# Kernel optimization log

Hardware: AMD Instinct MI355X
Metric: run time of the kernel (lower is better)

The kernel has to match this reference:

```python
import jax, jax.numpy as jnp
import numpy as np

N_NODES = 50000
N_EDGES = 800000
IN_FEATS = 256
HIDDEN = 256
NUM_CLASSES = 64


def setup_inputs() -> dict:
    key = jax.random.key(0)
    k1, k2, k3, k4 = jax.random.split(key, 4)
    features = jax.random.normal(k1, (N_NODES, IN_FEATS), dtype=jnp.float32)
    edge_index = jax.random.randint(k2, (2, N_EDGES), 0, N_NODES, dtype=jnp.int32)
    W1 = jax.random.normal(k3, (IN_FEATS, HIDDEN), dtype=jnp.float32) * (1.0 / np.sqrt(IN_FEATS))
    b1 = jnp.zeros((HIDDEN,), dtype=jnp.float32)
    W2 = jax.random.normal(k4, (HIDDEN, NUM_CLASSES), dtype=jnp.float32) * (1.0 / np.sqrt(HIDDEN))
    b2 = jnp.zeros((NUM_CLASSES,), dtype=jnp.float32)
    return {"features": features, "edge_index": edge_index, "W1": W1, "b1": b1, "W2": W2, "b2": b2}


def reference(features, edge_index, W1, b1, W2, b2):
    # Two-layer GCN: h = A_hat @ relu(A_hat @ X W1 + b1) W2 + b2
    # A_hat uses symmetric degree normalization 1/sqrt(d_src * d_dst)
    N = features.shape[0]
    src, dst = edge_index[0], edge_index[1]
    ones = jnp.ones((src.shape[0],), dtype=features.dtype)
    deg_out = jax.ops.segment_sum(ones, src, num_segments=N)  # out-degree per node
    deg_in = jax.ops.segment_sum(ones, dst, num_segments=N)   # in-degree per node
    inv_sqrt_out = jax.lax.rsqrt(jnp.maximum(deg_out, 1.0))
    inv_sqrt_in = jax.lax.rsqrt(jnp.maximum(deg_in, 1.0))
    edge_norm = (inv_sqrt_out[src] * inv_sqrt_in[dst])[:, None]  # [E,1]

    def gcn_layer(x, W, b):
        h = x @ W                      # transform first (reduces message width)
        msg = h[src] * edge_norm       # [E, out]
        agg = jax.ops.segment_sum(msg, dst, num_segments=N)
        return agg + b

    h = jax.nn.relu(gcn_layer(features, W1, b1))
    return gcn_layer(h, W2, b2)
```

## Files before the change

### kernel.cpp

```cpp
#include <hip/hip_runtime.h>

#define NN 50000
#define MPAD 50048
#define NE 800000
#define SCAN_BLOCKS 49

typedef short short8 __attribute__((ext_vector_type(8)));
typedef float f32x4 __attribute__((ext_vector_type(4)));

__device__ __forceinline__ unsigned short f2bf(float x) {
    unsigned u = __builtin_bit_cast(unsigned, x);
    u += 0x7FFFu + ((u >> 16) & 1u);
    return (unsigned short)(u >> 16);
}
__device__ __forceinline__ float bf2f(unsigned short h) {
    unsigned u = ((unsigned)h) << 16;
    return __builtin_bit_cast(float, u);
}
__device__ __forceinline__ void gld16(const void* g, void* l) {
    __builtin_amdgcn_global_load_lds(
        (const __attribute__((address_space(1))) unsigned int*)g,
        (__attribute__((address_space(3))) unsigned int*)l, 16, 0, 0);
}
__device__ __forceinline__ void nt_store8(void* p, ushort4 v) {
    __builtin_nontemporal_store(__builtin_bit_cast(unsigned long long, v),
                                (unsigned long long*)p);
}


__global__ __launch_bounds__(256) void count_kernel(const int* __restrict__ src,
    const int* __restrict__ dst, int* __restrict__ cnt_out, int* __restrict__ cnt_in, int E)
{
    int e = blockIdx.x * 256 + threadIdx.x;
    if (e < E) {
        atomicAdd(&cnt_out[src[e]], 1);
        atomicAdd(&cnt_in[dst[e]], 1);
    }
}

__global__ __launch_bounds__(256) void scanA_kernel(const int* __restrict__ cnt,
    int* __restrict__ bsum)
{
    __shared__ int sm[256];
    int b = blockIdx.x, tid = threadIdx.x;
    int base = b * 1024 + tid * 4;
    int s = 0;
    #pragma unroll
    for (int i = 0; i < 4; ++i) {
        int idx = base + i;
        if (idx < NN) s += cnt[idx];
    }
    sm[tid] = s;
    __syncthreads();
    for (int off = 128; off > 0; off >>= 1) {
        if (tid < off) sm[tid] += sm[tid + off];
        __syncthreads();
    }
    if (tid == 0) bsum[b] = sm[0];
}

__global__ __launch_bounds__(64) void scanB_kernel(const int* __restrict__ bsum,
    int* __restrict__ bexcl)
{
    int tid = threadIdx.x;
    int orig = (tid < SCAN_BLOCKS) ? bsum[tid] : 0;
    int v = orig;
    #pragma unroll
    for (int off = 1; off < 64; off <<= 1) {
        int u = __shfl_up(v, off, 64);
        if (tid >= off) v += u;
    }
    if (tid < SCAN_BLOCKS) bexcl[tid] = v - orig;
}

__global__ __launch_bounds__(256) void scanC_kernel(const int* __restrict__ cnt,
    const int* __restrict__ cnt_out, const int* __restrict__ bexcl,
    int* __restrict__ rs, float* __restrict__ inv_out, float* __restrict__ inv_in)
{
    __shared__ int wsum[4];
    int b = blockIdx.x, tid = threadIdx.x;
    int lane = tid & 63, wv = tid >> 6;
    int base = b * 1024 + tid * 4;
    int v[4]; int s = 0;
    #pragma unroll
    for (int i = 0; i < 4; ++i) {
        int idx = base + i;
        v[i] = (idx < NN) ? cnt[idx] : 0;
        s += v[i];
    }
    int inc = s;
    #pragma unroll
    for (int off = 1; off < 64; off <<= 1) {
        int u = __shfl_up(inc, off, 64);
        if (lane >= off) inc += u;
    }
    if (lane == 63) wsum[wv] = inc;
    __syncthreads();
    int wo = 0;
    for (int i = 0; i < wv; ++i) wo += wsum[i];
    int run = wo + (inc - s) + bexcl[b];
    #pragma unroll
    for (int i = 0; i < 4; ++i) {
        int idx = base + i;
        if (idx < NN) {
            rs[idx] = run; run += v[i];
            inv_in[idx]  = rsqrtf(fmaxf((float)v[i], 1.0f));
            inv_out[idx] = rsqrtf(fmaxf((float)cnt_out[idx], 1.0f));
        }
    }
}

__global__ __launch_bounds__(256) void fill_kernel(const int* __restrict__ src,
    const int* __restrict__ dst, int* __restrict__ rs, int* __restrict__ csr_src, int E)
{
    int e = blockIdx.x * 256 + threadIdx.x;
    if (e < E) {
        int slot = atomicAdd(&rs[dst[e]], 1);
        csr_src[slot] = src[e];
    }
}

__global__ __launch_bounds__(256) void splitX_kernel(const float* __restrict__ X,
    unsigned short* __restrict__ Xh, unsigned short* __restrict__ Xl)
{
    int i = blockIdx.x * 256 + threadIdx.x;
    if (i >= NN * 32) return;
    int r = i >> 5, c = i & 31;
    const float* src = X + (size_t)r * 256 + c * 8;
    float4 a0 = *(const float4*)src;
    float4 a1 = *(const float4*)(src + 4);
    float xs[8] = {a0.x, a0.y, a0.z, a0.w, a1.x, a1.y, a1.z, a1.w};
    short8 hv, lv;
    #pragma unroll
    for (int t = 0; t < 8; ++t) {
        unsigned short h = f2bf(xs[t]);
        hv[t] = (short)h;
        lv[t] = (short)f2bf(xs[t] - bf2f(h));
    }
    size_t off = (size_t)r * 256 + (c >> 3) * 64 + (((c & 7) ^ (r & 7)) * 8);
    *(short8*)&Xh[off] = hv;
    *(short8*)&Xl[off] = lv;
}

__global__ __launch_bounds__(256) void splitW_kernel(const float* __restrict__ W1,
    const float* __restrict__ W2, unsigned short* __restrict__ W1T,
    unsigned short* __restrict__ W2T)
{
    int i = blockIdx.x * 256 + threadIdx.x;
    const float* W; unsigned short* BT; int N; int ii;
    if (i < 256 * 32) { W = W1; BT = W1T; N = 256; ii = i; }
    else if (i < 256 * 32 + 64 * 32) { W = W2; BT = W2T; N = 64; ii = i - 256 * 32; }
    else return;
    int col = ii >> 5, kc = ii & 31;
    #pragma unroll
    for (int j = 0; j < 8; ++j) {
        float x = W[(size_t)(kc * 8 + j) * N + col];
        unsigned short h = f2bf(x);
        BT[(size_t)col * 512 + kc * 8 + j] = h;
        BT[(size_t)col * 512 + 256 + kc * 8 + j] = f2bf(x - bf2f(h));
    }
}

template<int BN>
__global__ __launch_bounds__(256) void gemm_sp_kernel(
    const unsigned short* __restrict__ Ah, const unsigned short* __restrict__ Al,
    const unsigned short* __restrict__ BT, const float* __restrict__ inv_out,
    unsigned short* __restrict__ C, int M, int Ntot)
{
    constexpr int WN = BN / 2;
    constexpr int NF = WN / 16;
    __shared__ unsigned short Ash[128 * 64];
    __shared__ unsigned short Asl[128 * 64];
    const int tid = threadIdx.x;
    const int w = tid >> 6, lane = tid & 63;
    const int wm = w >> 1, wn = w & 1;
    const int r = lane & 15, kg = lane >> 4;
    const int rowbase = blockIdx.x * 128;
    const int colbase = blockIdx.y * BN;

    f32x4 acc[4][NF] = {};

    for (int kb = 0; kb < 4; ++kb) {
        #pragma unroll
        for (int i = 0; i < 4; ++i) {
            int ct = (w * 4 + i) * 64 + lane;
            int row = ct >> 3, c = ct & 7;
            size_t goff = (size_t)(rowbase + row) * 256 + kb * 64 + c * 8;
            gld16(Ah + goff, (unsigned short*)Ash + (size_t)ct * 8);
            gld16(Al + goff, (unsigned short*)Asl + (size_t)ct * 8);
        }
        __syncthreads();
        #pragma unroll
        for (int ks = 0; ks < 2; ++ks) {
            short8 ahf[4], alf[4];
            #pragma unroll
            for (int mf = 0; mf < 4; ++mf) {
                int row = wm * 64 + mf * 16 + r;
                int lo = row * 64 + (((ks * 4 + kg) ^ (row & 7)) * 8);
                ahf[mf] = *(const short8*)&Ash[lo];
                alf[mf] = *(const short8*)&Asl[lo];
            }
            #pragma unroll
            for (int nf = 0; nf < NF; ++nf) {
                const unsigned short* bp = BT
                    + (size_t)(colbase + wn * WN + nf * 16 + r) * 512
                    + kb * 64 + ks * 32 + kg * 8;
                short8 bh = *(const short8*)bp;
                short8 bl = *(const short8*)(bp + 256);
                #pragma unroll
                for (int mf = 0; mf < 4; ++mf) {
                    acc[mf][nf] = __builtin_amdgcn_mfma_f32_16x16x32_bf16(ahf[mf], bh, acc[mf][nf], 0, 0, 0);
                    acc[mf][nf] = __builtin_amdgcn_mfma_f32_16x16x32_bf16(alf[mf], bh, acc[mf][nf], 0, 0, 0);
                    acc[mf][nf] = __builtin_amdgcn_mfma_f32_16x16x32_bf16(ahf[mf], bl, acc[mf][nf], 0, 0, 0);
                }
            }
        }
        __syncthreads();
    }

    #pragma unroll
    for (int mf = 0; mf < 4; ++mf) {
        #pragma unroll
        for (int reg = 0; reg < 4; ++reg) {
            int orow = rowbase + wm * 64 + mf * 16 + kg * 4 + reg;
            if (orow >= M) continue;
            float sc = inv_out[orow];
            #pragma unroll
            for (int nf = 0; nf < NF; ++nf) {
                int ocol = colbase + wn * WN + nf * 16 + r;
                C[(size_t)orow * Ntot + ocol] = f2bf(acc[mf][nf][reg] * sc);
            }
        }
    }
}

__global__ __launch_bounds__(256) void gather256_kernel(const unsigned short* __restrict__ t1,
    const int* __restrict__ csr_src, const int* __restrict__ rs,
    const float* __restrict__ inv_in, const float* __restrict__ b1,
    unsigned short* __restrict__ Ah2, unsigned short* __restrict__ Al2)
{
    int n = (int)((blockIdx.x * 256 + threadIdx.x) >> 6);
    int lane = threadIdx.x & 63;
    if (n >= NN) return;
    int begin = (n == 0) ? 0 : rs[n - 1];
    int end = rs[n];
    float a0 = 0.f, a1 = 0.f, a2 = 0.f, a3 = 0.f;
    int j = begin;
    for (; j + 8 <= end; j += 8) {
        int s0 = csr_src[j],     s1 = csr_src[j + 1], s2 = csr_src[j + 2], s3 = csr_src[j + 3];
        int s4 = csr_src[j + 4], s5 = csr_src[j + 5], s6 = csr_src[j + 6], s7 = csr_src[j + 7];
        ushort4 v0 = *(const ushort4*)&t1[(size_t)s0 * 256 + lane * 4];
        ushort4 v1 = *(const ushort4*)&t1[(size_t)s1 * 256 + lane * 4];
        ushort4 v2 = *(const ushort4*)&t1[(size_t)s2 * 256 + lane * 4];
        ushort4 v3 = *(const ushort4*)&t1[(size_t)s3 * 256 + lane * 4];
        ushort4 v4 = *(const ushort4*)&t1[(size_t)s4 * 256 + lane * 4];
        ushort4 v5 = *(const ushort4*)&t1[(size_t)s5 * 256 + lane * 4];
        ushort4 v6 = *(const ushort4*)&t1[(size_t)s6 * 256 + lane * 4];
        ushort4 v7 = *(const ushort4*)&t1[(size_t)s7 * 256 + lane * 4];
        a0 += bf2f(v0.x); a1 += bf2f(v0.y); a2 += bf2f(v0.z); a3 += bf2f(v0.w);
        a0 += bf2f(v1.x); a1 += bf2f(v1.y); a2 += bf2f(v1.z); a3 += bf2f(v1.w);
        a0 += bf2f(v2.x); a1 += bf2f(v2.y); a2 += bf2f(v2.z); a3 += bf2f(v2.w);
        a0 += bf2f(v3.x); a1 += bf2f(v3.y); a2 += bf2f(v3.z); a3 += bf2f(v3.w);
        a0 += bf2f(v4.x); a1 += bf2f(v4.y); a2 += bf2f(v4.z); a3 += bf2f(v4.w);
        a0 += bf2f(v5.x); a1 += bf2f(v5.y); a2 += bf2f(v5.z); a3 += bf2f(v5.w);
        a0 += bf2f(v6.x); a1 += bf2f(v6.y); a2 += bf2f(v6.z); a3 += bf2f(v6.w);
        a0 += bf2f(v7.x); a1 += bf2f(v7.y); a2 += bf2f(v7.z); a3 += bf2f(v7.w);
    }
    for (; j < end; ++j) {
        int s = csr_src[j];
        ushort4 v = *(const ushort4*)&t1[(size_t)s * 256 + lane * 4];
        a0 += bf2f(v.x); a1 += bf2f(v.y); a2 += bf2f(v.z); a3 += bf2f(v.w);
    }
    float win = inv_in[n];
    int f0 = lane * 4;
    float4 bb = *(const float4*)&b1[f0];
    float x0 = fmaxf(fmaf(a0, win, bb.x), 0.f);
    float x1 = fmaxf(fmaf(a1, win, bb.y), 0.f);
    float x2 = fmaxf(fmaf(a2, win, bb.z), 0.f);
    float x3 = fmaxf(fmaf(a3, win, bb.w), 0.f);
    unsigned short h0 = f2bf(x0), h1 = f2bf(x1), h2 = f2bf(x2), h3 = f2bf(x3);
    ushort4 hv = {h0, h1, h2, h3};
    ushort4 lv = {f2bf(x0 - bf2f(h0)), f2bf(x1 - bf2f(h1)),
                  f2bf(x2 - bf2f(h2)), f2bf(x3 - bf2f(h3))};
    int kb = f0 >> 6, c = (f0 >> 3) & 7, e = f0 & 7;
    size_t off = (size_t)n * 256 + kb * 64 + ((c ^ (n & 7)) * 8) + e;
    nt_store8(&Ah2[off], hv);
    nt_store8(&Al2[off], lv);
}

__global__ __launch_bounds__(256) void gather64_kernel(const unsigned short* __restrict__ t2,
    const int* __restrict__ csr_src, const int* __restrict__ rs,
    const float* __restrict__ inv_in, const float* __restrict__ b2,
    float* __restrict__ out)
{
    int n = (int)((blockIdx.x * 256 + threadIdx.x) >> 6);
    int lane = threadIdx.x & 63;
    if (n >= NN) return;
    int begin = (n == 0) ? 0 : rs[n - 1];
    int end = rs[n];
    float acc = 0.f;
    int j = begin;
    for (; j + 8 <= end; j += 8) {
        int s0 = csr_src[j],     s1 = csr_src[j + 1], s2 = csr_src[j + 2], s3 = csr_src[j + 3];
        int s4 = csr_src[j + 4], s5 = csr_src[j + 5], s6 = csr_src[j + 6], s7 = csr_src[j + 7];
        float v0 = bf2f(t2[(size_t)s0 * 64 + lane]);
        float v1 = bf2f(t2[(size_t)s1 * 64 + lane]);
        float v2 = bf2f(t2[(size_t)s2 * 64 + lane]);
        float v3 = bf2f(t2[(size_t)s3 * 64 + lane]);
        float v4 = bf2f(t2[(size_t)s4 * 64 + lane]);
        float v5 = bf2f(t2[(size_t)s5 * 64 + lane]);
        float v6 = bf2f(t2[(size_t)s6 * 64 + lane]);
        float v7 = bf2f(t2[(size_t)s7 * 64 + lane]);
        acc += v0; acc += v1; acc += v2; acc += v3;
        acc += v4; acc += v5; acc += v6; acc += v7;
    }
    for (; j < end; ++j) {
        int s = csr_src[j];
        acc += bf2f(t2[(size_t)s * 64 + lane]);
    }
    float o = fmaf(acc, inv_in[n], b2[lane]);
    __builtin_nontemporal_store(o, &out[(size_t)n * 64 + lane]);
}

extern "C" void kernel_launch(void* const* d_in, const int* in_sizes, int n_in,
                              void* d_out, int out_size, void* d_ws, size_t ws_size,
                              hipStream_t stream)
{
    const float* features = (const float*)d_in[0];
    const int*   edge_index = (const int*)d_in[1];
    const float* W1 = (const float*)d_in[2];
    const float* b1 = (const float*)d_in[3];
    const float* W2 = (const float*)d_in[4];
    const float* b2 = (const float*)d_in[5];
    float* out = (float*)d_out;
    const int* src = edge_index;
    const int* dst = edge_index + NE;

    char* p = (char*)d_ws;
    int* cnt_out = (int*)p;            p += (size_t)NN * 4;
    int* cnt_in  = (int*)p;            p += (size_t)NN * 4;
    float* inv_out = (float*)p;        p += (size_t)NN * 4;
    float* inv_in  = (float*)p;        p += (size_t)NN * 4;
    int* rs      = (int*)p;            p += (size_t)NN * 4;
    int* csr_src = (int*)p;            p += (size_t)NE * 4;
    int* bsum    = (int*)p;            p += 64 * 4;
    int* bexcl   = (int*)p;            p += 64 * 4;
    unsigned short* W1T = (unsigned short*)p;  p += (size_t)256 * 512 * 2;
    unsigned short* W2T = (unsigned short*)p;  p += (size_t)64 * 512 * 2;
    unsigned short* Xh  = (unsigned short*)p;  p += (size_t)MPAD * 256 * 2;
    unsigned short* Xl  = (unsigned short*)p;  p += (size_t)MPAD * 256 * 2;
    unsigned short* t1  = (unsigned short*)p;  p += (size_t)NN * 256 * 2;
    unsigned short* Ah2 = (unsigned short*)p;  p += (size_t)MPAD * 256 * 2;
    unsigned short* Al2 = (unsigned short*)p;  p += (size_t)MPAD * 256 * 2;
    unsigned short* t2  = (unsigned short*)p;  p += (size_t)NN * 64 * 2;

    hipMemsetAsync(cnt_out, 0, 2 * (size_t)NN * sizeof(int), stream);

    count_kernel<<<(NE + 255) / 256, 256, 0, stream>>>(src, dst, cnt_out, cnt_in, NE);
    scanA_kernel<<<SCAN_BLOCKS, 256, 0, stream>>>(cnt_in, bsum);
    scanB_kernel<<<1, 64, 0, stream>>>(bsum, bexcl);
    scanC_kernel<<<SCAN_BLOCKS, 256, 0, stream>>>(cnt_in, cnt_out, bexcl, rs, inv_out, inv_in);
    fill_kernel<<<(NE + 255) / 256, 256, 0, stream>>>(src, dst, rs, csr_src, NE);

    splitX_kernel<<<(NN * 32 + 255) / 256, 256, 0, stream>>>(features, Xh, Xl);
    splitW_kernel<<<(320 * 32 + 255) / 256, 256, 0, stream>>>(W1, W2, W1T, W2T);

    gemm_sp_kernel<128><<<dim3(MPAD / 128, 2), 256, 0, stream>>>(
        Xh, Xl, W1T, inv_out, t1, NN, 256);

    gather256_kernel<<<(NN * 64 + 255) / 256, 256, 0, stream>>>(
        t1, csr_src, rs, inv_in, b1, Ah2, Al2);

    gemm_sp_kernel<64><<<dim3(MPAD / 128, 1), 256, 0, stream>>>(
        Ah2, Al2, W2T, inv_out, t2, NN, 64);

    gather64_kernel<<<(NN * 64 + 255) / 256, 256, 0, stream>>>(
        t2, csr_src, rs, inv_in, b2, out);
}
```

Before: 340.6 us.

## Fuse fp32-to-bf16 split of X into first GEMM and stage B in LDS

The separate splitX pass, which wrote hi/lo bf16 copies of the features to global memory, is removed. The first GEMM now loads fp32 rows directly, splits them into hi/lo in registers and writes them swizzled into LDS. Both GEMMs also stage the swizzled transposed weight tiles in LDS instead of reading B fragments straight from global memory each k-step. This cuts a full write and re-read of a large intermediate buffer plus one launch, at the cost of more LDS per block and synchronous register-path loads for A in GEMM1.

New measurement: 300.6 us. -11.7%, faster.

```diff
diff --git a/kernel.cpp b/kernel.cpp
--- a/kernel.cpp
+++ b/kernel.cpp
@@ -120,28 +120,6 @@
     }
 }
 
-__global__ __launch_bounds__(256) void splitX_kernel(const float* __restrict__ X,
-    unsigned short* __restrict__ Xh, unsigned short* __restrict__ Xl)
-{
-    int i = blockIdx.x * 256 + threadIdx.x;
-    if (i >= NN * 32) return;
-    int r = i >> 5, c = i & 31;
-    const float* src = X + (size_t)r * 256 + c * 8;
-    float4 a0 = *(const float4*)src;
-    float4 a1 = *(const float4*)(src + 4);
-    float xs[8] = {a0.x, a0.y, a0.z, a0.w, a1.x, a1.y, a1.z, a1.w};
-    short8 hv, lv;
-    #pragma unroll
-    for (int t = 0; t < 8; ++t) {
-        unsigned short h = f2bf(xs[t]);
-        hv[t] = (short)h;
-        lv[t] = (short)f2bf(xs[t] - bf2f(h));
-    }
-    size_t off = (size_t)r * 256 + (c >> 3) * 64 + (((c & 7) ^ (r & 7)) * 8);
-    *(short8*)&Xh[off] = hv;
-    *(short8*)&Xl[off] = lv;
-}
-
 __global__ __launch_bounds__(256) void splitW_kernel(const float* __restrict__ W1,
     const float* __restrict__ W2, unsigned short* __restrict__ W1T,
     unsigned short* __restrict__ W2T)
@@ -152,25 +130,29 @@
     else if (i < 256 * 32 + 64 * 32) { W = W2; BT = W2T; N = 64; ii = i - 256 * 32; }
     else return;
     int col = ii >> 5, kc = ii & 31;
+    short8 hv, lv;
     #pragma unroll
     for (int j = 0; j < 8; ++j) {
         float x = W[(size_t)(kc * 8 + j) * N + col];
         unsigned short h = f2bf(x);
-        BT[(size_t)col * 512 + kc * 8 + j] = h;
-        BT[(size_t)col * 512 + 256 + kc * 8 + j] = f2bf(x - bf2f(h));
-    }
-}
-
-template<int BN>
-__global__ __launch_bounds__(256) void gemm_sp_kernel(
-    const unsigned short* __restrict__ Ah, const unsigned short* __restrict__ Al,
+        hv[j] = (short)h;
+        lv[j] = (short)f2bf(x - bf2f(h));
+    }
+    size_t base = (size_t)col * 512;
+    size_t o = (kc >> 3) * 64 + (((kc & 7) ^ (col & 7)) * 8);
+    *(short8*)&BT[base + o] = hv;
+    *(short8*)&BT[base + 256 + o] = lv;
+}
+
+__global__ __launch_bounds__(256) void gemm1_fuse_kernel(const float* __restrict__ X,
     const unsigned short* __restrict__ BT, const float* __restrict__ inv_out,
-    unsigned short* __restrict__ C, int M, int Ntot)
-{
-    constexpr int WN = BN / 2;
-    constexpr int NF = WN / 16;
+    unsigned short* __restrict__ C, int M)
+{
+    constexpr int BN = 128, WN = 64, NF = 4;
     __shared__ unsigned short Ash[128 * 64];
     __shared__ unsigned short Asl[128 * 64];
+    __shared__ unsigned short Bsh[BN * 64];
+    __shared__ unsigned short Bsl[BN * 64];
     const int tid = threadIdx.x;
     const int w = tid >> 6, lane = tid & 63;
     const int wm = w >> 1, wn = w & 1;
@@ -185,9 +167,29 @@
         for (int i = 0; i < 4; ++i) {
             int ct = (w * 4 + i) * 64 + lane;
             int row = ct >> 3, c = ct & 7;
-            size_t goff = (size_t)(rowbase + row) * 256 + kb * 64 + c * 8;
-            gld16(Ah + goff, (unsigned short*)Ash + (size_t)ct * 8);
-            gld16(Al + goff, (unsigned short*)Asl + (size_t)ct * 8);
+            int grow = rowbase + row; if (grow >= NN) grow = NN - 1;
+            const float* sp = X + (size_t)grow * 256 + kb * 64 + c * 8;
+            float4 x0 = *(const float4*)sp;
+            float4 x1 = *(const float4*)(sp + 4);
+            float xs[8] = {x0.x, x0.y, x0.z, x0.w, x1.x, x1.y, x1.z, x1.w};
+            short8 hv, lv;
+            #pragma unroll
+            for (int t = 0; t < 8; ++t) {
+                unsigned short h = f2bf(xs[t]);
+                hv[t] = (short)h;
+                lv[t] = (short)f2bf(xs[t] - bf2f(h));
+            }
+            int dsto = row * 64 + ((c ^ (row & 7)) * 8);
+            *(short8*)&Ash[dsto] = hv;
+            *(short8*)&Asl[dsto] = lv;
+        }
+        #pragma unroll
+        for (int i = 0; i < 4; ++i) {
+            int ct = (w * 4 + i) * 64 + lane;
+            int col = ct >> 3, c = ct & 7;
+            size_t goff = (size_t)(colbase + col) * 512 + kb * 64 + c * 8;
+            gld16(BT + goff, (unsigned short*)Bsh + (size_t)ct * 8);
+            gld16(BT + goff + 256, (unsigned short*)Bsl + (size_t)ct * 8);
         }
         __syncthreads();
         #pragma unroll
@@ -202,11 +204,10 @@
             }
             #pragma unroll
             for (int nf = 0; nf < NF; ++nf) {
-                const unsigned short* bp = BT
-                    + (size_t)(colbase + wn * WN + nf * 16 + r) * 512
-                    + kb * 64 + ks * 32 + kg * 8;
-                short8 bh = *(const short8*)bp;
-                short8 bl = *(const short8*)(bp + 256);
+                int col = wn * WN + nf * 16 + r;
+                int lo = col * 64 + (((ks * 4 + kg) ^ (col & 7)) * 8);
+                short8 bh = *(const short8*)&Bsh[lo];
+                short8 bl = *(const short8*)&Bsl[lo];
                 #pragma unroll
                 for (int mf = 0; mf < 4; ++mf) {
                     acc[mf][nf] = __builtin_amdgcn_mfma_f32_16x16x32_bf16(ahf[mf], bh, acc[mf][nf], 0, 0, 0);
@@ -228,7 +229,86 @@
             #pragma unroll
             for (int nf = 0; nf < NF; ++nf) {
                 int ocol = colbase + wn * WN + nf * 16 + r;
-                C[(size_t)orow * Ntot + ocol] = f2bf(acc[mf][nf][reg] * sc);
+                C[(size_t)orow * 256 + ocol] = f2bf(acc[mf][nf][reg] * sc);
+            }
+        }
+    }
+}
+
+__global__ __launch_bounds__(256) void gemm2_kernel(
+    const unsigned short* __restrict__ Ah, const unsigned short* __restrict__ Al,
+    const unsigned short* __restrict__ BT, const float* __restrict__ inv_out,
+    unsigned short* __restrict__ C, int M)
+{
+    constexpr int BN = 64, WN = 32, NF = 2, BI = 2;
+    __shared__ unsigned short Ash[128 * 64];
+    __shared__ unsigned short Asl[128 * 64];
+    __shared__ unsigned short Bsh[BN * 64];
+    __shared__ unsigned short Bsl[BN * 64];
+    const int tid = threadIdx.x;
+    const int w = tid >> 6, lane = tid & 63;
+    const int wm = w >> 1, wn = w & 1;
+    const int r = lane & 15, kg = lane >> 4;
+    const int rowbase = blockIdx.x * 128;
+
+    f32x4 acc[4][NF] = {};
+
+    for (int kb = 0; kb < 4; ++kb) {
+        #pragma unroll
+        for (int i = 0; i < 4; ++i) {
+            int ct = (w * 4 + i) * 64 + lane;
+            int row = ct >> 3, c = ct & 7;
+            size_t goff = (size_t)(rowbase + row) * 256 + kb * 64 + c * 8;
+            gld16(Ah + goff, (unsigned short*)Ash + (size_t)ct * 8);
+            gld16(Al + goff, (unsigned short*)Asl + (size_t)ct * 8);
+        }
+        #pragma unroll
+        for (int i = 0; i < BI; ++i) {
+            int ct = (w * BI + i) * 64 + lane;
+            int col = ct >> 3, c = ct & 7;
+            size_t goff = (size_t)col * 512 + kb * 64 + c * 8;
+            gld16(BT + goff, (unsigned short*)Bsh + (size_t)ct * 8);
+            gld16(BT + goff + 256, (unsigned short*)Bsl + (size_t)ct * 8);
+        }
+        __syncthreads();
+        #pragma unroll
+        for (int ks = 0; ks < 2; ++ks) {
+            short8 ahf[4], alf[4];
+            #pragma unroll
+            for (int mf = 0; mf < 4; ++mf) {
+                int row = wm * 64 + mf * 16 + r;
+                int lo = row * 64 + (((ks * 4 + kg) ^ (row & 7)) * 8);
+                ahf[mf] = *(const short8*)&Ash[lo];
+                alf[mf] = *(const short8*)&Asl[lo];
+            }
+            #pragma unroll
+            for (int nf = 0; nf < NF; ++nf) {
+                int col = wn * WN + nf * 16 + r;
+                int lo = col * 64 + (((ks * 4 + kg) ^ (col & 7)) * 8);
+                short8 bh = *(const short8*)&Bsh[lo];
+                short8 bl = *(const short8*)&Bsl[lo];
+                #pragma unroll
+                for (int mf = 0; mf < 4; ++mf) {
+                    acc[mf][nf] = __builtin_amdgcn_mfma_f32_16x16x32_bf16(ahf[mf], bh, acc[mf][nf], 0, 0, 0);
+                    acc[mf][nf] = __builtin_amdgcn_mfma_f32_16x16x32_bf16(alf[mf], bh, acc[mf][nf], 0, 0, 0);
+                    acc[mf][nf] = __builtin_amdgcn_mfma_f32_16x16x32_bf16(ahf[mf], bl, acc[mf][nf], 0, 0, 0);
+                }
+            }
+        }
+        __syncthreads();
+    }
+
+    #pragma unroll
+    for (int mf = 0; mf < 4; ++mf) {
+        #pragma unroll
+        for (int reg = 0; reg < 4; ++reg) {
+            int orow = rowbase + wm * 64 + mf * 16 + kg * 4 + reg;
+            if (orow >= M) continue;
+            float sc = inv_out[orow];
+            #pragma unroll
+            for (int nf = 0; nf < NF; ++nf) {
+                int ocol = wn * WN + nf * 16 + r;
+                C[(size_t)orow * 64 + ocol] = f2bf(acc[mf][nf][reg] * sc);
             }
         }
     }
@@ -347,8 +427,6 @@
     int* bexcl   = (int*)p;            p += 64 * 4;
     unsigned short* W1T = (unsigned short*)p;  p += (size_t)256 * 512 * 2;
     unsigned short* W2T = (unsigned short*)p;  p += (size_t)64 * 512 * 2;
-    unsigned short* Xh  = (unsigned short*)p;  p += (size_t)MPAD * 256 * 2;
-    unsigned short* Xl  = (unsigned short*)p;  p += (size_t)MPAD * 256 * 2;
     unsigned short* t1  = (unsigned short*)p;  p += (size_t)NN * 256 * 2;
     unsigned short* Ah2 = (unsigned short*)p;  p += (size_t)MPAD * 256 * 2;
     unsigned short* Al2 = (unsigned short*)p;  p += (size_t)MPAD * 256 * 2;
@@ -362,17 +440,16 @@
     scanC_kernel<<<SCAN_BLOCKS, 256, 0, stream>>>(cnt_in, cnt_out, bexcl, rs, inv_out, inv_in);
     fill_kernel<<<(NE + 255) / 256, 256, 0, stream>>>(src, dst, rs, csr_src, NE);
 
-    splitX_kernel<<<(NN * 32 + 255) / 256, 256, 0, stream>>>(features, Xh, Xl);
     splitW_kernel<<<(320 * 32 + 255) / 256, 256, 0, stream>>>(W1, W2, W1T, W2T);
 
-    gemm_sp_kernel<128><<<dim3(MPAD / 128, 2), 256, 0, stream>>>(
-        Xh, Xl, W1T, inv_out, t1, NN, 256);
+    gemm1_fuse_kernel<<<dim3(MPAD / 128, 2), 256, 0, stream>>>(
+        features, W1T, inv_out, t1, NN);
 
     gather256_kernel<<<(NN * 64 + 255) / 256, 256, 0, stream>>>(
         t1, csr_src, rs, inv_in, b1, Ah2, Al2);
 
-    gemm_sp_kernel<64><<<dim3(MPAD / 128, 1), 256, 0, stream>>>(
-        Ah2, Al2, W2T, inv_out, t2, NN, 64);
+    gemm2_kernel<<<MPAD / 128, 256, 0, stream>>>(
+        Ah2, Al2, W2T, inv_out, t2, NN);
 
     gather64_kernel<<<(NN * 64 + 255) / 256, 256, 0, stream>>>(
         t2, csr_src, rs, inv_in, b2, out);
```
